# Kernel tuning notes

Measured on AMD Instinct MI355X. Metric: run time of the kernel, lower is better.

The kernel has to match this reference:

```python
import jax, jax.numpy as jnp
import numpy as np

N_NODES = 50000
N_EDGES = 640000
IN_CH, HID_CH, OUT_CH = 128, 128, 40


def setup_inputs() -> dict:
    key = jax.random.key(0)
    k1, k2, k3, k4 = jax.random.split(key, 4)
    x = jax.random.normal(k1, (N_NODES, IN_CH), dtype=jnp.float32)
    edge_index = jax.random.randint(k2, (2, N_EDGES), 0, N_NODES, dtype=jnp.int64)
    # Glorot-ish scaled weights
    W1 = jax.random.normal(k3, (IN_CH, HID_CH), dtype=jnp.float32) * (1.0 / np.sqrt(IN_CH))
    b1 = jnp.zeros((HID_CH,), dtype=jnp.float32)
    W2 = jax.random.normal(k4, (HID_CH, OUT_CH), dtype=jnp.float32) * (1.0 / np.sqrt(HID_CH))
    b2 = jnp.zeros((OUT_CH,), dtype=jnp.float32)
    return {"x": x, "edge_index": edge_index, "W1": W1, "b1": b1, "W2": W2, "b2": b2}


def gcn_conv(x, src, dst, W, b, n_nodes):
    """PyG-style GCNConv: self-loops + symmetric normalization + linear + bias.
    src/dst already include self-loop edges."""
    deg = jax.ops.segment_sum(jnp.ones_like(dst, dtype=x.dtype), dst, num_segments=n_nodes)
    dinv = jnp.where(deg > 0, jax.lax.rsqrt(deg), 0.0)          # deg^{-1/2}, 0 for isolated
    norm = dinv[src] * dinv[dst]                                 # [E+N]
    xw = x @ W                                                   # [N, F_out] dense GEMM
    msgs = xw[src] * norm[:, None]                               # gather + scale  [E+N, F_out]
    agg = jax.ops.segment_sum(msgs, dst, num_segments=n_nodes)   # scatter-add
    return agg + b


def reference(x, edge_index, W1, b1, W2, b2):
    n_nodes = x.shape[0]
    loops = jnp.arange(n_nodes, dtype=edge_index.dtype)
    src = jnp.concatenate([edge_index[0], loops])
    dst = jnp.concatenate([edge_index[1], loops])
    h = jax.nn.relu(gcn_conv(x, src, dst, W1, b1, n_nodes))
    # dropout is identity in eval mode (deterministic reference)
    return gcn_conv(h, src, dst, W2, b2, n_nodes)
```

## Files before the change

### kernel.cpp

```cpp
#include <hip/hip_runtime.h>
#include <cstdint>

#define NN 50000
#define NE 640000

typedef unsigned short ushort_t;

__device__ __forceinline__ ushort_t f2bf(float f) {
    unsigned int b = __float_as_uint(f);
    return (ushort_t)((b + 0x7FFF + ((b >> 16) & 1)) >> 16);
}
__device__ __forceinline__ float bf2f(ushort_t u) {
    return __uint_as_float(((unsigned int)u) << 16);
}


__global__ void hist_kernel(const int* __restrict__ dst, int* __restrict__ cnt) {
    int i = blockIdx.x * 256 + threadIdx.x;
    if (i < NE) atomicAdd(&cnt[dst[i]], 1);
}

__global__ void scan_block(const int* __restrict__ in, int* __restrict__ out,
                           int* __restrict__ partials, int n) {
    __shared__ int sm[256];
    int t = threadIdx.x;
    int gid = blockIdx.x * 256 + t;
    int v = (gid < n) ? in[gid] : 0;
    sm[t] = v;
    __syncthreads();
#pragma unroll
    for (int off = 1; off < 256; off <<= 1) {
        int add = (t >= off) ? sm[t - off] : 0;
        __syncthreads();
        sm[t] += add;
        __syncthreads();
    }
    if (gid < n) out[gid] = sm[t] - v;
    if (t == 255) partials[blockIdx.x] = sm[255];
}

__global__ void scan_partials(int* __restrict__ p, int nb) {
    __shared__ int sm[256];
    int t = threadIdx.x;
    int v = (t < nb) ? p[t] : 0;
    sm[t] = v;
    __syncthreads();
#pragma unroll
    for (int off = 1; off < 256; off <<= 1) {
        int add = (t >= off) ? sm[t - off] : 0;
        __syncthreads();
        sm[t] += add;
        __syncthreads();
    }
    if (t < nb) p[t] = sm[t] - v;
}

__global__ void finalize_offsets(int* __restrict__ offs, const int* __restrict__ partials,
                                 int* __restrict__ cursor, const int* __restrict__ cnt,
                                 float* __restrict__ dinv, int n) {
    int gid = blockIdx.x * 256 + threadIdx.x;
    if (gid < n) {
        int v = offs[gid] + partials[blockIdx.x];
        offs[gid] = v;
        cursor[gid] = v;
        dinv[gid] = rsqrtf((float)cnt[gid] + 1.0f);
    }
}

__global__ void csr_fill(const int* __restrict__ ei, const float* __restrict__ dinv,
                         int* __restrict__ cursor, int2* __restrict__ csr) {
    int e = blockIdx.x * 256 + threadIdx.x;
    if (e < NE) {
        int s = ei[e], d = ei[NE + e];
        int pos = atomicAdd(&cursor[d], 1);
        csr[pos] = make_int2(s, __float_as_int(dinv[s] * dinv[d]));
    }
}


__global__ __launch_bounds__(256) void gemm_k128_bf16out(const float* __restrict__ A,
                                                         const float* __restrict__ B,
                                                         ushort_t* __restrict__ C,
                                                         int M, int N) {
    __shared__ float As[64][68];
    __shared__ __align__(16) float Bs[64][64];
    const int t  = threadIdx.x;
    const int m0 = blockIdx.x * 64;
    const int n0 = blockIdx.y * 64;
    const int tx = t & 15, ty = t >> 4;

    float acc[4][4] = {};

    for (int ks = 0; ks < 2; ++ks) {
#pragma unroll
        for (int i = 0; i < 4; ++i) {
            int idx = i * 256 + t;
            int r = idx >> 4, c4 = idx & 15;
            int gm = m0 + r;
            float4 v = make_float4(0.f, 0.f, 0.f, 0.f);
            if (gm < M) v = *reinterpret_cast<const float4*>(&A[(size_t)gm * 128 + ks * 64 + c4 * 4]);
            As[r][c4 * 4 + 0] = v.x;
            As[r][c4 * 4 + 1] = v.y;
            As[r][c4 * 4 + 2] = v.z;
            As[r][c4 * 4 + 3] = v.w;
        }
#pragma unroll
        for (int i = 0; i < 4; ++i) {
            int idx = i * 256 + t;
            int k = idx >> 4, c4 = idx & 15;
            int gk = ks * 64 + k;
            int gn = n0 + c4 * 4;
            float4 v;
            v.x = (gn + 0 < N) ? B[(size_t)gk * N + gn + 0] : 0.f;
            v.y = (gn + 1 < N) ? B[(size_t)gk * N + gn + 1] : 0.f;
            v.z = (gn + 2 < N) ? B[(size_t)gk * N + gn + 2] : 0.f;
            v.w = (gn + 3 < N) ? B[(size_t)gk * N + gn + 3] : 0.f;
            *reinterpret_cast<float4*>(&Bs[k][c4 * 4]) = v;
        }
        __syncthreads();

#pragma unroll 8
        for (int k = 0; k < 64; ++k) {
            float a0 = As[ty * 4 + 0][k];
            float a1 = As[ty * 4 + 1][k];
            float a2 = As[ty * 4 + 2][k];
            float a3 = As[ty * 4 + 3][k];
            float4 b = *reinterpret_cast<const float4*>(&Bs[k][tx * 4]);
            acc[0][0] += a0 * b.x; acc[0][1] += a0 * b.y; acc[0][2] += a0 * b.z; acc[0][3] += a0 * b.w;
            acc[1][0] += a1 * b.x; acc[1][1] += a1 * b.y; acc[1][2] += a1 * b.z; acc[1][3] += a1 * b.w;
            acc[2][0] += a2 * b.x; acc[2][1] += a2 * b.y; acc[2][2] += a2 * b.z; acc[2][3] += a2 * b.w;
            acc[3][0] += a3 * b.x; acc[3][1] += a3 * b.y; acc[3][2] += a3 * b.z; acc[3][3] += a3 * b.w;
        }
        __syncthreads();
    }

#pragma unroll
    for (int i = 0; i < 4; ++i) {
        int gm = m0 + ty * 4 + i;
        if (gm >= M) continue;
        int gn = n0 + tx * 4;
        if (gn + 3 < N) {
            ushort4 o;
            o.x = f2bf(acc[i][0]); o.y = f2bf(acc[i][1]);
            o.z = f2bf(acc[i][2]); o.w = f2bf(acc[i][3]);
            *reinterpret_cast<ushort4*>(&C[(size_t)gm * N + gn]) = o;
        } else {
#pragma unroll
            for (int j = 0; j < 4; ++j)
                if (gn + j < N) C[(size_t)gm * N + gn + j] = f2bf(acc[i][j]);
        }
    }
}


__global__ __launch_bounds__(256) void gather128(const int* __restrict__ offs,
                                                 const int* __restrict__ ends,
                                                 const int2* __restrict__ csr,
                                                 const ushort_t* __restrict__ H1,
                                                 const float* __restrict__ dinv,
                                                 const float* __restrict__ b1,
                                                 float* __restrict__ h) {
    const int c = (threadIdx.x & 31) * 4;
    const int n = (blockIdx.x * 256 + threadIdx.x) >> 5;
    const int beg = offs[n], end = ends[n];
    float4 acc = make_float4(0.f, 0.f, 0.f, 0.f);
    int j = beg;
    const int n4end = beg + ((end - beg) & ~3);
    for (; j < n4end; j += 4) {
        int2 p0 = csr[j + 0], p1 = csr[j + 1], p2 = csr[j + 2], p3 = csr[j + 3];
        ushort4 v0 = *reinterpret_cast<const ushort4*>(H1 + (size_t)p0.x * 128 + c);
        ushort4 v1 = *reinterpret_cast<const ushort4*>(H1 + (size_t)p1.x * 128 + c);
        ushort4 v2 = *reinterpret_cast<const ushort4*>(H1 + (size_t)p2.x * 128 + c);
        ushort4 v3 = *reinterpret_cast<const ushort4*>(H1 + (size_t)p3.x * 128 + c);
        float w0 = __int_as_float(p0.y), w1 = __int_as_float(p1.y);
        float w2 = __int_as_float(p2.y), w3 = __int_as_float(p3.y);
        acc.x += bf2f(v0.x) * w0 + bf2f(v1.x) * w1 + bf2f(v2.x) * w2 + bf2f(v3.x) * w3;
        acc.y += bf2f(v0.y) * w0 + bf2f(v1.y) * w1 + bf2f(v2.y) * w2 + bf2f(v3.y) * w3;
        acc.z += bf2f(v0.z) * w0 + bf2f(v1.z) * w1 + bf2f(v2.z) * w2 + bf2f(v3.z) * w3;
        acc.w += bf2f(v0.w) * w0 + bf2f(v1.w) * w1 + bf2f(v2.w) * w2 + bf2f(v3.w) * w3;
    }
    for (; j < end; ++j) {
        int2 p = csr[j];
        float w = __int_as_float(p.y);
        ushort4 v = *reinterpret_cast<const ushort4*>(H1 + (size_t)p.x * 128 + c);
        acc.x += bf2f(v.x) * w; acc.y += bf2f(v.y) * w;
        acc.z += bf2f(v.z) * w; acc.w += bf2f(v.w) * w;
    }
    float di = dinv[n];
    float sl = di * di;
    ushort4 sv = *reinterpret_cast<const ushort4*>(H1 + (size_t)n * 128 + c);
    float4 bv = *reinterpret_cast<const float4*>(b1 + c);
    float4 r;
    r.x = fmaxf(fmaf(bf2f(sv.x), sl, acc.x + bv.x), 0.f);
    r.y = fmaxf(fmaf(bf2f(sv.y), sl, acc.y + bv.y), 0.f);
    r.z = fmaxf(fmaf(bf2f(sv.z), sl, acc.z + bv.z), 0.f);
    r.w = fmaxf(fmaf(bf2f(sv.w), sl, acc.w + bv.w), 0.f);
    *reinterpret_cast<float4*>(h + (size_t)n * 128 + c) = r;
}


__global__ __launch_bounds__(256) void gather40(const int* __restrict__ offs,
                                                const int* __restrict__ ends,
                                                const int2* __restrict__ csr,
                                                const ushort_t* __restrict__ H2,
                                                const float* __restrict__ dinv,
                                                const float* __restrict__ b2,
                                                float* __restrict__ out) {
    int idx = blockIdx.x * 256 + threadIdx.x;
    if (idx >= NN * 10) return;
    const int n = idx / 10;
    const int c = (idx - n * 10) * 4;
    const int beg = offs[n], end = ends[n];
    float4 acc = make_float4(0.f, 0.f, 0.f, 0.f);
    int j = beg;
    const int n4end = beg + ((end - beg) & ~3);
    for (; j < n4end; j += 4) {
        int2 p0 = csr[j + 0], p1 = csr[j + 1], p2 = csr[j + 2], p3 = csr[j + 3];
        ushort4 v0 = *reinterpret_cast<const ushort4*>(H2 + (size_t)p0.x * 40 + c);
        ushort4 v1 = *reinterpret_cast<const ushort4*>(H2 + (size_t)p1.x * 40 + c);
        ushort4 v2 = *reinterpret_cast<const ushort4*>(H2 + (size_t)p2.x * 40 + c);
        ushort4 v3 = *reinterpret_cast<const ushort4*>(H2 + (size_t)p3.x * 40 + c);
        float w0 = __int_as_float(p0.y), w1 = __int_as_float(p1.y);
        float w2 = __int_as_float(p2.y), w3 = __int_as_float(p3.y);
        acc.x += bf2f(v0.x) * w0 + bf2f(v1.x) * w1 + bf2f(v2.x) * w2 + bf2f(v3.x) * w3;
        acc.y += bf2f(v0.y) * w0 + bf2f(v1.y) * w1 + bf2f(v2.y) * w2 + bf2f(v3.y) * w3;
        acc.z += bf2f(v0.z) * w0 + bf2f(v1.z) * w1 + bf2f(v2.z) * w2 + bf2f(v3.z) * w3;
        acc.w += bf2f(v0.w) * w0 + bf2f(v1.w) * w1 + bf2f(v2.w) * w2 + bf2f(v3.w) * w3;
    }
    for (; j < end; ++j) {
        int2 p = csr[j];
        float w = __int_as_float(p.y);
        ushort4 v = *reinterpret_cast<const ushort4*>(H2 + (size_t)p.x * 40 + c);
        acc.x += bf2f(v.x) * w; acc.y += bf2f(v.y) * w;
        acc.z += bf2f(v.z) * w; acc.w += bf2f(v.w) * w;
    }
    float di = dinv[n];
    float sl = di * di;
    ushort4 sv = *reinterpret_cast<const ushort4*>(H2 + (size_t)n * 40 + c);
    float4 bv = *reinterpret_cast<const float4*>(b2 + c);
    float4 r;
    r.x = fmaf(bf2f(sv.x), sl, acc.x + bv.x);
    r.y = fmaf(bf2f(sv.y), sl, acc.y + bv.y);
    r.z = fmaf(bf2f(sv.z), sl, acc.z + bv.z);
    r.w = fmaf(bf2f(sv.w), sl, acc.w + bv.w);
    *reinterpret_cast<float4*>(out + (size_t)n * 40 + c) = r;
}


extern "C" void kernel_launch(void* const* d_in, const int* in_sizes, int n_in,
                              void* d_out, int out_size, void* d_ws, size_t ws_size,
                              hipStream_t stream) {
    const float* x  = (const float*)d_in[0];
    const int*   ei = (const int*)d_in[1];
    const float* W1 = (const float*)d_in[2];
    const float* b1 = (const float*)d_in[3];
    const float* W2 = (const float*)d_in[4];
    const float* b2 = (const float*)d_in[5];
    float* out = (float*)d_out;

    int*      deg_i    = (int*)d_ws;
    float*    dinv     = (float*)d_ws + 50048;
    int*      offs     = (int*)d_ws + 100096;
    int*      cursor   = (int*)d_ws + 150144;
    int*      partials = (int*)d_ws + 200192;
    int2*     csr      = (int2*)((int*)d_ws + 200704);
    ushort_t* H1b      = (ushort_t*)((int*)d_ws + 1480704);
    float*    h        = (float*)d_ws + 4680704;
    ushort_t* H2b      = H1b;

    const int NB = (NN + 255) / 256;

    hipMemsetAsync(deg_i, 0, NN * sizeof(int), stream);
    hist_kernel<<<(NE + 255) / 256, 256, 0, stream>>>(ei + NE, deg_i);
    scan_block<<<NB, 256, 0, stream>>>(deg_i, offs, partials, NN);
    scan_partials<<<1, 256, 0, stream>>>(partials, NB);
    finalize_offsets<<<NB, 256, 0, stream>>>(offs, partials, cursor, deg_i, dinv, NN);
    csr_fill<<<(NE + 255) / 256, 256, 0, stream>>>(ei, dinv, cursor, csr);

    gemm_k128_bf16out<<<dim3((NN + 63) / 64, 2), 256, 0, stream>>>(x, W1, H1b, NN, 128);
    gather128<<<NN * 32 / 256, 256, 0, stream>>>(offs, cursor, csr, H1b, dinv, b1, h);

    gemm_k128_bf16out<<<dim3((NN + 63) / 64, 1), 256, 0, stream>>>(h, W2, H2b, NN, 40);
    gather40<<<(NN * 10 + 255) / 256, 256, 0, stream>>>(offs, cursor, csr, H2b, dinv, b2, out);
}
```

Baseline: 243.6 us.

## Fold source-side degree scaling into GEMM epilogue and shrink CSR to src indices

Factors the symmetric normalization dinv[s]*dinv[d] so the GEMM epilogue scales each row by dinv[src] and the gather applies dinv[dst] once at the end. The CSR then stores only 4-byte source indices instead of int2 pairs, which halves edge-list traffic in both gathers and drops the per-edge multiplies and the dinv gathers in csr_fill. The hist and csr_fill kernels also process four edges per thread with fixed strides that hard-code NE. Rounding changes slightly because the scaled values are rounded to bf16 before aggregation.

Result: no change. 244.8 us (+0.5%).

```diff
diff --git a/kernel.cpp b/kernel.cpp
--- a/kernel.cpp
+++ b/kernel.cpp
@@ -16,8 +16,12 @@
 
 
 __global__ void hist_kernel(const int* __restrict__ dst, int* __restrict__ cnt) {
-    int i = blockIdx.x * 256 + threadIdx.x;
-    if (i < NE) atomicAdd(&cnt[dst[i]], 1);
+    int tid = blockIdx.x * 256 + threadIdx.x;
+#pragma unroll
+    for (int k = 0; k < 4; ++k) {
+        int e = tid + k * 160000;
+        atomicAdd(&cnt[dst[e]], 1);
+    }
 }
 
 __global__ void scan_block(const int* __restrict__ in, int* __restrict__ out,
@@ -67,21 +71,24 @@
     }
 }
 
-__global__ void csr_fill(const int* __restrict__ ei, const float* __restrict__ dinv,
-                         int* __restrict__ cursor, int2* __restrict__ csr) {
-    int e = blockIdx.x * 256 + threadIdx.x;
-    if (e < NE) {
+__global__ void csr_fill(const int* __restrict__ ei, int* __restrict__ cursor,
+                         int* __restrict__ csr_src) {
+    int tid = blockIdx.x * 256 + threadIdx.x;
+#pragma unroll
+    for (int k = 0; k < 4; ++k) {
+        int e = tid + k * 160000;
         int s = ei[e], d = ei[NE + e];
         int pos = atomicAdd(&cursor[d], 1);
-        csr[pos] = make_int2(s, __float_as_int(dinv[s] * dinv[d]));
-    }
-}
-
-
-__global__ __launch_bounds__(256) void gemm_k128_bf16out(const float* __restrict__ A,
-                                                         const float* __restrict__ B,
-                                                         ushort_t* __restrict__ C,
-                                                         int M, int N) {
+        csr_src[pos] = s;
+    }
+}
+
+
+__global__ __launch_bounds__(256) void gemm_k128_scaled(const float* __restrict__ A,
+                                                        const float* __restrict__ B,
+                                                        const float* __restrict__ dinv,
+                                                        ushort_t* __restrict__ C,
+                                                        int M, int N) {
     __shared__ float As[64][68];
     __shared__ __align__(16) float Bs[64][64];
     const int t  = threadIdx.x;
@@ -138,16 +145,17 @@
     for (int i = 0; i < 4; ++i) {
         int gm = m0 + ty * 4 + i;
         if (gm >= M) continue;
+        float s = dinv[gm];
         int gn = n0 + tx * 4;
         if (gn + 3 < N) {
             ushort4 o;
-            o.x = f2bf(acc[i][0]); o.y = f2bf(acc[i][1]);
-            o.z = f2bf(acc[i][2]); o.w = f2bf(acc[i][3]);
+            o.x = f2bf(acc[i][0] * s); o.y = f2bf(acc[i][1] * s);
+            o.z = f2bf(acc[i][2] * s); o.w = f2bf(acc[i][3] * s);
             *reinterpret_cast<ushort4*>(&C[(size_t)gm * N + gn]) = o;
         } else {
 #pragma unroll
             for (int j = 0; j < 4; ++j)
-                if (gn + j < N) C[(size_t)gm * N + gn + j] = f2bf(acc[i][j]);
+                if (gn + j < N) C[(size_t)gm * N + gn + j] = f2bf(acc[i][j] * s);
         }
     }
 }
@@ -155,8 +163,8 @@
 
 __global__ __launch_bounds__(256) void gather128(const int* __restrict__ offs,
                                                  const int* __restrict__ ends,
-                                                 const int2* __restrict__ csr,
-                                                 const ushort_t* __restrict__ H1,
+                                                 const int* __restrict__ csr_src,
+                                                 const ushort_t* __restrict__ Hs,
                                                  const float* __restrict__ dinv,
                                                  const float* __restrict__ b1,
                                                  float* __restrict__ h) {
@@ -167,42 +175,39 @@
     int j = beg;
     const int n4end = beg + ((end - beg) & ~3);
     for (; j < n4end; j += 4) {
-        int2 p0 = csr[j + 0], p1 = csr[j + 1], p2 = csr[j + 2], p3 = csr[j + 3];
-        ushort4 v0 = *reinterpret_cast<const ushort4*>(H1 + (size_t)p0.x * 128 + c);
-        ushort4 v1 = *reinterpret_cast<const ushort4*>(H1 + (size_t)p1.x * 128 + c);
-        ushort4 v2 = *reinterpret_cast<const ushort4*>(H1 + (size_t)p2.x * 128 + c);
-        ushort4 v3 = *reinterpret_cast<const ushort4*>(H1 + (size_t)p3.x * 128 + c);
-        float w0 = __int_as_float(p0.y), w1 = __int_as_float(p1.y);
-        float w2 = __int_as_float(p2.y), w3 = __int_as_float(p3.y);
-        acc.x += bf2f(v0.x) * w0 + bf2f(v1.x) * w1 + bf2f(v2.x) * w2 + bf2f(v3.x) * w3;
-        acc.y += bf2f(v0.y) * w0 + bf2f(v1.y) * w1 + bf2f(v2.y) * w2 + bf2f(v3.y) * w3;
-        acc.z += bf2f(v0.z) * w0 + bf2f(v1.z) * w1 + bf2f(v2.z) * w2 + bf2f(v3.z) * w3;
-        acc.w += bf2f(v0.w) * w0 + bf2f(v1.w) * w1 + bf2f(v2.w) * w2 + bf2f(v3.w) * w3;
+        int s0 = csr_src[j + 0], s1 = csr_src[j + 1];
+        int s2 = csr_src[j + 2], s3 = csr_src[j + 3];
+        ushort4 v0 = *reinterpret_cast<const ushort4*>(Hs + (size_t)s0 * 128 + c);
+        ushort4 v1 = *reinterpret_cast<const ushort4*>(Hs + (size_t)s1 * 128 + c);
+        ushort4 v2 = *reinterpret_cast<const ushort4*>(Hs + (size_t)s2 * 128 + c);
+        ushort4 v3 = *reinterpret_cast<const ushort4*>(Hs + (size_t)s3 * 128 + c);
+        acc.x += bf2f(v0.x) + bf2f(v1.x) + bf2f(v2.x) + bf2f(v3.x);
+        acc.y += bf2f(v0.y) + bf2f(v1.y) + bf2f(v2.y) + bf2f(v3.y);
+        acc.z += bf2f(v0.z) + bf2f(v1.z) + bf2f(v2.z) + bf2f(v3.z);
+        acc.w += bf2f(v0.w) + bf2f(v1.w) + bf2f(v2.w) + bf2f(v3.w);
     }
     for (; j < end; ++j) {
-        int2 p = csr[j];
-        float w = __int_as_float(p.y);
-        ushort4 v = *reinterpret_cast<const ushort4*>(H1 + (size_t)p.x * 128 + c);
-        acc.x += bf2f(v.x) * w; acc.y += bf2f(v.y) * w;
-        acc.z += bf2f(v.z) * w; acc.w += bf2f(v.w) * w;
+        int s = csr_src[j];
+        ushort4 v = *reinterpret_cast<const ushort4*>(Hs + (size_t)s * 128 + c);
+        acc.x += bf2f(v.x); acc.y += bf2f(v.y);
+        acc.z += bf2f(v.z); acc.w += bf2f(v.w);
     }
     float di = dinv[n];
-    float sl = di * di;
-    ushort4 sv = *reinterpret_cast<const ushort4*>(H1 + (size_t)n * 128 + c);
+    ushort4 sv = *reinterpret_cast<const ushort4*>(Hs + (size_t)n * 128 + c);
     float4 bv = *reinterpret_cast<const float4*>(b1 + c);
     float4 r;
-    r.x = fmaxf(fmaf(bf2f(sv.x), sl, acc.x + bv.x), 0.f);
-    r.y = fmaxf(fmaf(bf2f(sv.y), sl, acc.y + bv.y), 0.f);
-    r.z = fmaxf(fmaf(bf2f(sv.z), sl, acc.z + bv.z), 0.f);
-    r.w = fmaxf(fmaf(bf2f(sv.w), sl, acc.w + bv.w), 0.f);
+    r.x = fmaxf(fmaf(di, acc.x + bf2f(sv.x), bv.x), 0.f);
+    r.y = fmaxf(fmaf(di, acc.y + bf2f(sv.y), bv.y), 0.f);
+    r.z = fmaxf(fmaf(di, acc.z + bf2f(sv.z), bv.z), 0.f);
+    r.w = fmaxf(fmaf(di, acc.w + bf2f(sv.w), bv.w), 0.f);
     *reinterpret_cast<float4*>(h + (size_t)n * 128 + c) = r;
 }
 
 
 __global__ __launch_bounds__(256) void gather40(const int* __restrict__ offs,
                                                 const int* __restrict__ ends,
-                                                const int2* __restrict__ csr,
-                                                const ushort_t* __restrict__ H2,
+                                                const int* __restrict__ csr_src,
+                                                const ushort_t* __restrict__ Hs,
                                                 const float* __restrict__ dinv,
                                                 const float* __restrict__ b2,
                                                 float* __restrict__ out) {
@@ -215,34 +220,31 @@
     int j = beg;
     const int n4end = beg + ((end - beg) & ~3);
     for (; j < n4end; j += 4) {
-        int2 p0 = csr[j + 0], p1 = csr[j + 1], p2 = csr[j + 2], p3 = csr[j + 3];
-        ushort4 v0 = *reinterpret_cast<const ushort4*>(H2 + (size_t)p0.x * 40 + c);
-        ushort4 v1 = *reinterpret_cast<const ushort4*>(H2 + (size_t)p1.x * 40 + c);
-        ushort4 v2 = *reinterpret_cast<const ushort4*>(H2 + (size_t)p2.x * 40 + c);
-        ushort4 v3 = *reinterpret_cast<const ushort4*>(H2 + (size_t)p3.x * 40 + c);
-        float w0 = __int_as_float(p0.y), w1 = __int_as_float(p1.y);
-        float w2 = __int_as_float(p2.y), w3 = __int_as_float(p3.y);
-        acc.x += bf2f(v0.x) * w0 + bf2f(v1.x) * w1 + bf2f(v2.x) * w2 + bf2f(v3.x) * w3;
-        acc.y += bf2f(v0.y) * w0 + bf2f(v1.y) * w1 + bf2f(v2.y) * w2 + bf2f(v3.y) * w3;
-        acc.z += bf2f(v0.z) * w0 + bf2f(v1.z) * w1 + bf2f(v2.z) * w2 + bf2f(v3.z) * w3;
-        acc.w += bf2f(v0.w) * w0 + bf2f(v1.w) * w1 + bf2f(v2.w) * w2 + bf2f(v3.w) * w3;
+        int s0 = csr_src[j + 0], s1 = csr_src[j + 1];
+        int s2 = csr_src[j + 2], s3 = csr_src[j + 3];
+        ushort4 v0 = *reinterpret_cast<const ushort4*>(Hs + (size_t)s0 * 40 + c);
+        ushort4 v1 = *reinterpret_cast<const ushort4*>(Hs + (size_t)s1 * 40 + c);
+        ushort4 v2 = *reinterpret_cast<const ushort4*>(Hs + (size_t)s2 * 40 + c);
+        ushort4 v3 = *reinterpret_cast<const ushort4*>(Hs + (size_t)s3 * 40 + c);
+        acc.x += bf2f(v0.x) + bf2f(v1.x) + bf2f(v2.x) + bf2f(v3.x);
+        acc.y += bf2f(v0.y) + bf2f(v1.y) + bf2f(v2.y) + bf2f(v3.y);
+        acc.z += bf2f(v0.z) + bf2f(v1.z) + bf2f(v2.z) + bf2f(v3.z);
+        acc.w += bf2f(v0.w) + bf2f(v1.w) + bf2f(v2.w) + bf2f(v3.w);
     }
     for (; j < end; ++j) {
-        int2 p = csr[j];
-        float w = __int_as_float(p.y);
-        ushort4 v = *reinterpret_cast<const ushort4*>(H2 + (size_t)p.x * 40 + c);
-        acc.x += bf2f(v.x) * w; acc.y += bf2f(v.y) * w;
-        acc.z += bf2f(v.z) * w; acc.w += bf2f(v.w) * w;
+        int s = csr_src[j];
+        ushort4 v = *reinterpret_cast<const ushort4*>(Hs + (size_t)s * 40 + c);
+        acc.x += bf2f(v.x); acc.y += bf2f(v.y);
+        acc.z += bf2f(v.z); acc.w += bf2f(v.w);
     }
     float di = dinv[n];
-    float sl = di * di;
-    ushort4 sv = *reinterpret_cast<const ushort4*>(H2 + (size_t)n * 40 + c);
+    ushort4 sv = *reinterpret_cast<const ushort4*>(Hs + (size_t)n * 40 + c);
     float4 bv = *reinterpret_cast<const float4*>(b2 + c);
     float4 r;
-    r.x = fmaf(bf2f(sv.x), sl, acc.x + bv.x);
-    r.y = fmaf(bf2f(sv.y), sl, acc.y + bv.y);
-    r.z = fmaf(bf2f(sv.z), sl, acc.z + bv.z);
-    r.w = fmaf(bf2f(sv.w), sl, acc.w + bv.w);
+    r.x = fmaf(di, acc.x + bf2f(sv.x), bv.x);
+    r.y = fmaf(di, acc.y + bf2f(sv.y), bv.y);
+    r.z = fmaf(di, acc.z + bf2f(sv.z), bv.z);
+    r.w = fmaf(di, acc.w + bf2f(sv.w), bv.w);
     *reinterpret_cast<float4*>(out + (size_t)n * 40 + c) = r;
 }
 
@@ -263,23 +265,23 @@
     int*      offs     = (int*)d_ws + 100096;
     int*      cursor   = (int*)d_ws + 150144;
     int*      partials = (int*)d_ws + 200192;
-    int2*     csr      = (int2*)((int*)d_ws + 200704);
-    ushort_t* H1b      = (ushort_t*)((int*)d_ws + 1480704);
-    float*    h        = (float*)d_ws + 4680704;
+    int*      csr_src  = (int*)d_ws + 200704;
+    ushort_t* H1b      = (ushort_t*)((int*)d_ws + 840704);
+    float*    h        = (float*)d_ws + 4040704;
     ushort_t* H2b      = H1b;
 
     const int NB = (NN + 255) / 256;
 
     hipMemsetAsync(deg_i, 0, NN * sizeof(int), stream);
-    hist_kernel<<<(NE + 255) / 256, 256, 0, stream>>>(ei + NE, deg_i);
+    hist_kernel<<<625, 256, 0, stream>>>(ei + NE, deg_i);
     scan_block<<<NB, 256, 0, stream>>>(deg_i, offs, partials, NN);
     scan_partials<<<1, 256, 0, stream>>>(partials, NB);
     finalize_offsets<<<NB, 256, 0, stream>>>(offs, partials, cursor, deg_i, dinv, NN);
-    csr_fill<<<(NE + 255) / 256, 256, 0, stream>>>(ei, dinv, cursor, csr);
-
-    gemm_k128_bf16out<<<dim3((NN + 63) / 64, 2), 256, 0, stream>>>(x, W1, H1b, NN, 128);
-    gather128<<<NN * 32 / 256, 256, 0, stream>>>(offs, cursor, csr, H1b, dinv, b1, h);
-
-    gemm_k128_bf16out<<<dim3((NN + 63) / 64, 1), 256, 0, stream>>>(h, W2, H2b, NN, 40);
-    gather40<<<(NN * 10 + 255) / 256, 256, 0, stream>>>(offs, cursor, csr, H2b, dinv, b2, out);
-}
+    csr_fill<<<625, 256, 0, stream>>>(ei, cursor, csr_src);
+
+    gemm_k128_scaled<<<dim3((NN + 63) / 64, 2), 256, 0, stream>>>(x, W1, dinv, H1b, NN, 128);
+    gather128<<<NN * 32 / 256, 256, 0, stream>>>(offs, cursor, csr_src, H1b, dinv, b1, h);
+
+    gemm_k128_scaled<<<dim3((NN + 63) / 64, 1), 256, 0, stream>>>(h, W2, dinv, H2b, NN, 40);
+    gather40<<<(NN * 10 + 255) / 256, 256, 0, stream>>>(offs, cursor, csr_src, H2b, dinv, b2, out);
+}
```
